# Optimization experiments

Hardware: AMD Instinct MI355X
Metric: run time of the kernel (lower is better)

## Reference

```python
import jax, jax.numpy as jnp
import numpy as np

EMBED = 1024
HEADS = 16
HEAD_DIM = EMBED // HEADS


def setup_inputs() -> dict:
    key = jax.random.key(0)
    ks = jax.random.split(key, 12)
    B, S, E = 2, 2048, EMBED
    scale = 1.0 / np.sqrt(E)
    inp = {
        "query": jax.random.normal(ks[0], (B, S, E), jnp.float32),
        "key": jax.random.normal(ks[1], (B, S, E), jnp.float32),
        "value": jax.random.normal(ks[2], (B, S, E), jnp.float32),
        "Wq": jax.random.normal(ks[3], (E, E), jnp.float32) * scale,
        "bq": jax.random.normal(ks[4], (E,), jnp.float32) * 0.01,
        "Wk": jax.random.normal(ks[5], (E, E), jnp.float32) * scale,
        "bk": jax.random.normal(ks[6], (E,), jnp.float32) * 0.01,
        "Wv": jax.random.normal(ks[7], (E, E), jnp.float32) * scale,
        "bv": jax.random.normal(ks[8], (E,), jnp.float32) * 0.01,
        "Wo": jax.random.normal(ks[9], (E, E), jnp.float32) * scale,
        "bo": jax.random.normal(ks[10], (E,), jnp.float32) * 0.01,
    }
    return inp


def reference(query, key, value, Wq, bq, Wk, bk, Wv, bv, Wo, bo):
    B, Sq, E = query.shape
    Sk = key.shape[1]
    H, D = HEADS, HEAD_DIM
    # QKV projections (torch Linear: x @ W.T + b)
    q = (query @ Wq.T + bq).reshape(B, Sq, H, D)
    k = (key @ Wk.T + bk).reshape(B, Sk, H, D)
    v = (value @ Wv.T + bv).reshape(B, Sk, H, D)
    # energy: [B, H, Sq, Sk]; note scale = 1/sqrt(embed_size), not head_dim
    energy = jnp.einsum("bqhd,bkhd->bhqk", q, k)
    scale = jnp.asarray(E, energy.dtype) ** 0.5
    attn = jax.nn.softmax(energy / scale, axis=-1)
    out = jnp.einsum("bhqk,bkhd->bqhd", attn, v).reshape(B, Sq, E)
    # fc_out (dropout is identity at eval)
    return out @ Wo.T + bo
```

## Files before the change

### kernel.cpp

```cpp
#include <hip/hip_runtime.h>
#include <hip/hip_bf16.h>

typedef __hip_bfloat16 bf16;
typedef short frag8 __attribute__((ext_vector_type(8)));
typedef _Float16 half4 __attribute__((ext_vector_type(4)));
typedef float f32x4 __attribute__((ext_vector_type(4)));

typedef __attribute__((address_space(3))) void lds_void;
typedef __attribute__((address_space(1))) const void gbl_void;

__device__ __forceinline__ void gld16(const void* g, void* l) {
  __builtin_amdgcn_global_load_lds((gbl_void*)g, (lds_void*)l, 16, 0, 0);
}

__device__ __forceinline__ unsigned short f2bf(float f) {
  union { float f; unsigned u; } x; x.f = f;
  unsigned r = x.u + 0x7FFFu + ((x.u >> 16) & 1u);
  return (unsigned short)(r >> 16);
}

#define QSCALE 0.0450842200278f
#define MFIX 4.0f

struct CvtArgs {
  const float4* src[4];
  ushort4* dst[4];
};
__global__ __launch_bounds__(256) void cvt_all(CvtArgs a) {
  const int t = blockIdx.y;
  const int i = blockIdx.x * 256 + threadIdx.x;
  float4 v = a.src[t][i];
  ushort4 o;
  o.x = f2bf(v.x); o.y = f2bf(v.y); o.z = f2bf(v.z); o.w = f2bf(v.w);
  a.dst[t][i] = o;
}

template<int MODE>
__global__ __launch_bounds__(256)
void gemm_bt(const void* __restrict__ A0, const void* __restrict__ A1, const void* __restrict__ A2,
             const bf16* __restrict__ W0, const bf16* __restrict__ W1, const bf16* __restrict__ W2,
             const float* __restrict__ b0, const float* __restrict__ b1, const float* __restrict__ b2,
             void* __restrict__ o0, void* __restrict__ o1, void* __restrict__ o2) {
  constexpr int NK = 1024;
  __shared__ __align__(16) bf16 As[2][128 * 32];
  __shared__ __align__(16) bf16 Bs[2][128 * 32];
  const int tid = threadIdx.x;
  const int wave = tid >> 6, lane = tid & 63, quad = lane >> 4, l16 = lane & 15;
  const int wm = wave >> 1, wn = wave & 1;
  const int bm = blockIdx.x, bn = blockIdx.y;

  const void* A = A0; const bf16* W = W0; const float* bias = b0; void* out = o0;
  int z = 0;
  if constexpr (MODE == 1) {
    z = blockIdx.z;
    if (z == 1) { A = A1; W = W1; bias = b1; out = o1; }
    else if (z == 2) { A = A2; W = W2; bias = b2; out = o2; }
  }

  f32x4 acc[4][4];
  #pragma unroll
  for (int i = 0; i < 4; ++i)
    #pragma unroll
    for (int j = 0; j < 4; ++j)
      acc[i][j] = (f32x4){0.f, 0.f, 0.f, 0.f};

  const bf16* Wb = W + (size_t)bn * 128 * NK;
  const int c0_ = tid & 3, r0_ = tid >> 2;

  auto stageW = [&](int k0, int buf) {
    #pragma unroll
    for (int is = 0; is < 2; ++is) {
      const int c = tid + is * 256;
      const int r = r0_ + is * 64;
      const int gc = (c0_ ^ (r & 3)) << 3;
      gld16(Wb + (size_t)r * NK + k0 + gc, (void*)(&Bs[buf][(size_t)c * 8]));
    }
  };

  const bf16* Ab16 = (const bf16*)A + (size_t)bm * 128 * NK;
  const float* Abf = (const float*)A + (size_t)bm * 128 * NK;
  float4 alo[2], ahi[2];
  auto loadA = [&](int k0, int buf) {
    if constexpr (MODE == 0) {
      #pragma unroll
      for (int is = 0; is < 2; ++is) {
        const int c = tid + is * 256;
        const int r = r0_ + is * 64;
        const int gc = (c0_ ^ (r & 3)) << 3;
        gld16(Ab16 + (size_t)r * NK + k0 + gc, (void*)(&As[buf][(size_t)c * 8]));
      }
    } else {
      #pragma unroll
      for (int is = 0; is < 2; ++is) {
        const int r = r0_ + is * 64;
        const int gc = (c0_ ^ (r & 3)) << 3;
        const float* p = Abf + (size_t)r * NK + k0 + gc;
        alo[is] = *(const float4*)p;
        ahi[is] = *(const float4*)(p + 4);
      }
    }
  };
  auto writeA = [&](int buf) {
    if constexpr (MODE == 1) {
      #pragma unroll
      for (int is = 0; is < 2; ++is) {
        const int c = tid + is * 256;
        ushort4 w0, w1;
        w0.x = f2bf(alo[is].x); w0.y = f2bf(alo[is].y); w0.z = f2bf(alo[is].z); w0.w = f2bf(alo[is].w);
        w1.x = f2bf(ahi[is].x); w1.y = f2bf(ahi[is].y); w1.z = f2bf(ahi[is].z); w1.w = f2bf(ahi[is].w);
        ushort* d = (ushort*)&As[buf][(size_t)c * 8];
        *(ushort4*)d = w0;
        *(ushort4*)(d + 4) = w1;
      }
    }
  };

  loadA(0, 0); stageW(0, 0); writeA(0);
  #pragma unroll 2
  for (int kt = 0; kt < 32; ++kt) {
    __syncthreads();
    if (kt < 31) { loadA((kt + 1) * 32, (kt + 1) & 1); stageW((kt + 1) * 32, (kt + 1) & 1); }
    const bf16* as_ = As[kt & 1];
    const bf16* bs_ = Bs[kt & 1];
    frag8 af[4], bfr[4];
    const int rc = (quad ^ (l16 & 3)) << 3;
    #pragma unroll
    for (int i = 0; i < 4; ++i)
      af[i] = *(const frag8*)&as_[(wm * 64 + i * 16 + l16) * 32 + rc];
    #pragma unroll
    for (int j = 0; j < 4; ++j)
      bfr[j] = *(const frag8*)&bs_[(wn * 64 + j * 16 + l16) * 32 + rc];
    #pragma unroll
    for (int i = 0; i < 4; ++i)
      #pragma unroll
      for (int j = 0; j < 4; ++j)
        acc[i][j] = __builtin_amdgcn_mfma_f32_16x16x32_bf16(af[i], bfr[j], acc[i][j], 0, 0, 0);
    if (kt < 31) writeA((kt + 1) & 1);
  }

  #pragma unroll
  for (int j = 0; j < 4; ++j) {
    const int col = bn * 128 + wn * 64 + j * 16 + l16;
    const float bv = bias[col];
    #pragma unroll
    for (int i = 0; i < 4; ++i) {
      #pragma unroll
      for (int r = 0; r < 4; ++r) {
        const int row = bm * 128 + wm * 64 + i * 16 + quad * 4 + r;
        float v = acc[i][j][r] + bv;
        if constexpr (MODE == 0) {
          ((float*)out)[(size_t)row * 1024 + col] = v;
        } else {
          const int b = row >> 11, s = row & 2047;
          const int hh = col >> 6, d = col & 63;
          const size_t bh = (size_t)(b * 16 + hh);
          if (z == 0) {
            v *= QSCALE;
            ((bf16*)out)[(bh * 2048 + s) * 64 + d] = __float2bfloat16(v);
          } else if (z == 1) {
            const int rr = s & 127;
            const size_t addr = bh * 131072 + (size_t)(s >> 7) * 8192 + (size_t)rr * 64
                              + (size_t)(((d >> 3) ^ (rr & 7)) << 3) + (d & 7);
            ((bf16*)out)[addr] = __float2bfloat16(v);
          } else {
            const int kvl = s & 127;
            const size_t addr = bh * 131072 + (size_t)(s >> 7) * 8192 + (size_t)d * 128
                              + (size_t)((((kvl >> 2) ^ (d & 15)) << 2)) + (kvl & 3);
            ((_Float16*)out)[addr] = (_Float16)v;
          }
        }
      }
    }
  }
}

__global__ __launch_bounds__(256)
void flash_attn(const bf16* __restrict__ Q, const bf16* __restrict__ K,
                const _Float16* __restrict__ Vt, bf16* __restrict__ ctx) {
  __shared__ __align__(16) bf16 Ks[2][128 * 64];
  __shared__ __align__(16) _Float16 Vs[2][64 * 128];
  const int tid = threadIdx.x;
  const int wave = tid >> 6, lane = tid & 63, quad = lane >> 4, l16 = lane & 15;
  const int bh = blockIdx.x, b = bh >> 4, h = bh & 15;
  const int q0 = blockIdx.y * 128 + wave * 32;
  const bf16* Qb = Q + (size_t)bh * 2048 * 64;
  const bf16* Kb = K + (size_t)bh * 131072;
  const _Float16* Vb = Vt + (size_t)bh * 131072;

  frag8 qf[2][2];
  #pragma unroll
  for (int qt = 0; qt < 2; ++qt)
    #pragma unroll
    for (int ks = 0; ks < 2; ++ks)
      qf[qt][ks] = *(const frag8*)(Qb + (size_t)(q0 + qt * 16 + l16) * 64 + ks * 32 + quad * 8);

  f32x4 rsv[2];
  f32x4 o[2][4];
  #pragma unroll
  for (int qt = 0; qt < 2; ++qt) {
    rsv[qt] = (f32x4){0.f, 0.f, 0.f, 0.f};
    #pragma unroll
    for (int dt = 0; dt < 4; ++dt)
      o[qt][dt] = (f32x4){0.f, 0.f, 0.f, 0.f};
  }

  const int xk = l16 & 7;

  auto stage = [&](int kt, int buf) {
    #pragma unroll
    for (int is = 0; is < 4; ++is) {
      const int c = tid + is * 256;
      gld16(Kb + (size_t)kt * 8192 + (size_t)c * 8, (void*)(&Ks[buf][(size_t)c * 8]));
      gld16(Vb + (size_t)kt * 8192 + (size_t)c * 8, (void*)(&Vs[buf][(size_t)c * 8]));
    }
  };

  stage(0, 0);
  #pragma unroll 2
  for (int kt = 0; kt < 16; ++kt) {
    __syncthreads();
    if (kt < 15) stage(kt + 1, (kt + 1) & 1);
    const bf16* ks_ = Ks[kt & 1];
    const _Float16* vs_ = Vs[kt & 1];

    f32x4 s[2][8];
    #pragma unroll
    for (int qt = 0; qt < 2; ++qt)
      #pragma unroll
      for (int jt = 0; jt < 8; ++jt)
        s[qt][jt] = (f32x4){-MFIX, -MFIX, -MFIX, -MFIX};
    #pragma unroll
    for (int ks = 0; ks < 2; ++ks) {
      frag8 kf[8];
      #pragma unroll
      for (int jt = 0; jt < 8; ++jt)
        kf[jt] = *(const frag8*)&ks_[(jt * 16 + l16) * 64 + (((ks * 4 + quad) ^ xk) << 3)];
      #pragma unroll
      for (int qt = 0; qt < 2; ++qt)
        #pragma unroll
        for (int jt = 0; jt < 8; ++jt)
          s[qt][jt] = __builtin_amdgcn_mfma_f32_16x16x32_bf16(kf[jt], qf[qt][ks], s[qt][jt], 0, 0, 0);
    }

    half4 pf[2][8];
    #pragma unroll
    for (int qt = 0; qt < 2; ++qt) {
      #pragma unroll
      for (int jt = 0; jt < 8; ++jt) {
        f32x4 p4;
        #pragma unroll
        for (int r = 0; r < 4; ++r)
          p4[r] = __builtin_amdgcn_exp2f(s[qt][jt][r]);
        rsv[qt] += p4;
        #pragma unroll
        for (int r = 0; r < 4; ++r)
          pf[qt][jt][r] = (_Float16)p4[r];
      }
    }

    #pragma unroll
    for (int jt = 0; jt < 8; ++jt) {
      half4 vf[4];
      #pragma unroll
      for (int dt = 0; dt < 4; ++dt)
        vf[dt] = *(const half4*)&vs_[(dt * 16 + l16) * 128 + (((jt * 4 + quad) ^ l16) << 2)];
      #pragma unroll
      for (int qt = 0; qt < 2; ++qt)
        #pragma unroll
        for (int dt = 0; dt < 4; ++dt)
          o[qt][dt] = __builtin_amdgcn_mfma_f32_16x16x16f16(vf[dt], pf[qt][jt], o[qt][dt], 0, 0, 0);
    }
  }

  #pragma unroll
  for (int qt = 0; qt < 2; ++qt) {
    float l = rsv[qt][0] + rsv[qt][1] + rsv[qt][2] + rsv[qt][3];
    l += __shfl_xor(l, 16, 64);
    l += __shfl_xor(l, 32, 64);
    const float inv = __builtin_amdgcn_rcpf(l);
    const int q = q0 + qt * 16 + l16;
    #pragma unroll
    for (int dt = 0; dt < 4; ++dt) {
      ushort4 w;
      w.x = f2bf(o[qt][dt][0] * inv);
      w.y = f2bf(o[qt][dt][1] * inv);
      w.z = f2bf(o[qt][dt][2] * inv);
      w.w = f2bf(o[qt][dt][3] * inv);
      const int d = dt * 16 + quad * 4;
      *(uint2*)&ctx[((size_t)(b * 2048 + q)) * 1024 + h * 64 + d] = *(uint2*)&w;
    }
  }
}

extern "C" void kernel_launch(void* const* d_in, const int* in_sizes, int n_in,
                              void* d_out, int out_size, void* d_ws, size_t ws_size,
                              hipStream_t stream) {
  const float* q_in = (const float*)d_in[0];
  const float* k_in = (const float*)d_in[1];
  const float* v_in = (const float*)d_in[2];
  const float* Wq = (const float*)d_in[3];
  const float* bq = (const float*)d_in[4];
  const float* Wk = (const float*)d_in[5];
  const float* bk = (const float*)d_in[6];
  const float* Wv = (const float*)d_in[7];
  const float* bv = (const float*)d_in[8];
  const float* Wo = (const float*)d_in[9];
  const float* bo = (const float*)d_in[10];

  char* ws = (char*)d_ws;
  const size_t MB = 1024 * 1024;
  bf16* Wqb = (bf16*)(ws + 0 * MB);
  bf16* Wkb = (bf16*)(ws + 2 * MB);
  bf16* Wvb = (bf16*)(ws + 4 * MB);
  bf16* Wob = (bf16*)(ws + 6 * MB);
  bf16* Qw  = (bf16*)(ws + 8 * MB);
  bf16* Kw  = (bf16*)(ws + 16 * MB);
  _Float16* Vtw = (_Float16*)(ws + 24 * MB);
  bf16* Ctx = (bf16*)(ws + 32 * MB);

  {
    CvtArgs a;
    a.src[0] = (const float4*)Wq; a.dst[0] = (ushort4*)Wqb;
    a.src[1] = (const float4*)Wk; a.dst[1] = (ushort4*)Wkb;
    a.src[2] = (const float4*)Wv; a.dst[2] = (ushort4*)Wvb;
    a.src[3] = (const float4*)Wo; a.dst[3] = (ushort4*)Wob;
    cvt_all<<<dim3(1024, 4), 256, 0, stream>>>(a);
  }

  gemm_bt<1><<<dim3(32, 8, 3), 256, 0, stream>>>(q_in, k_in, v_in, Wqb, Wkb, Wvb,
                                                 bq, bk, bv, Qw, Kw, (void*)Vtw);
  flash_attn<<<dim3(32, 16), 256, 0, stream>>>(Qw, Kw, Vtw, Ctx);
  gemm_bt<0><<<dim3(32, 8, 1), 256, 0, stream>>>(Ctx, nullptr, nullptr, Wob, nullptr, nullptr,
                                                 bo, nullptr, nullptr, d_out, nullptr, nullptr);
}
```

Measured before the change: 250.5 us.

## Halve output GEMM tile height and deepen fp32 A prefetch in QKV GEMM

The output projection GEMM now uses 64-row tiles with each wave owning 16 rows across all 128 columns, doubling the grid from 256 to 512 blocks so more of the GPU's compute units get work. The QKV projection GEMM gains a two-deep register prefetch of the fp32 A tiles, loading two k-steps ahead and converting one step ahead, to hide global-load latency behind the MFMAs. The trade-offs are less data reuse per block in the output GEMM and higher register pressure in the QKV GEMM.

```diff
diff --git a/kernel.cpp b/kernel.cpp
--- a/kernel.cpp
+++ b/kernel.cpp
@@ -42,7 +42,8 @@
              const float* __restrict__ b0, const float* __restrict__ b1, const float* __restrict__ b2,
              void* __restrict__ o0, void* __restrict__ o1, void* __restrict__ o2) {
   constexpr int NK = 1024;
-  __shared__ __align__(16) bf16 As[2][128 * 32];
+  constexpr int BM = (MODE == 1) ? 128 : 64;
+  __shared__ __align__(16) bf16 As[2][BM * 32];
   __shared__ __align__(16) bf16 Bs[2][128 * 32];
   const int tid = threadIdx.x;
   const int wave = tid >> 6, lane = tid & 63, quad = lane >> 4, l16 = lane & 15;
@@ -57,13 +58,6 @@
     else if (z == 2) { A = A2; W = W2; bias = b2; out = o2; }
   }
 
-  f32x4 acc[4][4];
-  #pragma unroll
-  for (int i = 0; i < 4; ++i)
-    #pragma unroll
-    for (int j = 0; j < 4; ++j)
-      acc[i][j] = (f32x4){0.f, 0.f, 0.f, 0.f};
-
   const bf16* Wb = W + (size_t)bn * 128 * NK;
   const int c0_ = tid & 3, r0_ = tid >> 2;
 
@@ -77,80 +71,116 @@
     }
   };
 
-  const bf16* Ab16 = (const bf16*)A + (size_t)bm * 128 * NK;
-  const float* Abf = (const float*)A + (size_t)bm * 128 * NK;
-  float4 alo[2], ahi[2];
-  auto loadA = [&](int k0, int buf) {
-    if constexpr (MODE == 0) {
-      #pragma unroll
-      for (int is = 0; is < 2; ++is) {
-        const int c = tid + is * 256;
-        const int r = r0_ + is * 64;
-        const int gc = (c0_ ^ (r & 3)) << 3;
-        gld16(Ab16 + (size_t)r * NK + k0 + gc, (void*)(&As[buf][(size_t)c * 8]));
-      }
-    } else {
+  const int rc = (quad ^ (l16 & 3)) << 3;
+
+  if constexpr (MODE == 0) {
+    const bf16* Ab16 = (const bf16*)A + (size_t)bm * 64 * NK;
+    f32x4 acc[8];
+    #pragma unroll
+    for (int j = 0; j < 8; ++j) acc[j] = (f32x4){0.f, 0.f, 0.f, 0.f};
+
+    auto stageA = [&](int k0, int buf) {
+      const int r = r0_;
+      const int gc = (c0_ ^ (r & 3)) << 3;
+      gld16(Ab16 + (size_t)r * NK + k0 + gc, (void*)(&As[buf][(size_t)tid * 8]));
+    };
+
+    stageA(0, 0); stageW(0, 0);
+    #pragma unroll 2
+    for (int kt = 0; kt < 32; ++kt) {
+      __syncthreads();
+      if (kt < 31) { stageA((kt + 1) * 32, (kt + 1) & 1); stageW((kt + 1) * 32, (kt + 1) & 1); }
+      const bf16* as_ = As[kt & 1];
+      const bf16* bs_ = Bs[kt & 1];
+      frag8 af = *(const frag8*)&as_[(wave * 16 + l16) * 32 + rc];
+      #pragma unroll
+      for (int j = 0; j < 8; ++j) {
+        frag8 bf_ = *(const frag8*)&bs_[(j * 16 + l16) * 32 + rc];
+        acc[j] = __builtin_amdgcn_mfma_f32_16x16x32_bf16(af, bf_, acc[j], 0, 0, 0);
+      }
+    }
+    #pragma unroll
+    for (int j = 0; j < 8; ++j) {
+      const int col = bn * 128 + j * 16 + l16;
+      const float bv = bias[col];
+      #pragma unroll
+      for (int r = 0; r < 4; ++r) {
+        const int row = bm * 64 + wave * 16 + quad * 4 + r;
+        ((float*)out)[(size_t)row * 1024 + col] = acc[j][r] + bv;
+      }
+    }
+  } else {
+    const float* Abf = (const float*)A + (size_t)bm * 128 * NK;
+    f32x4 acc[4][4];
+    #pragma unroll
+    for (int i = 0; i < 4; ++i)
+      #pragma unroll
+      for (int j = 0; j < 4; ++j)
+        acc[i][j] = (f32x4){0.f, 0.f, 0.f, 0.f};
+
+    float4 alo[2][2], ahi[2][2];
+    auto loadA = [&](int k0, int set) {
       #pragma unroll
       for (int is = 0; is < 2; ++is) {
         const int r = r0_ + is * 64;
         const int gc = (c0_ ^ (r & 3)) << 3;
         const float* p = Abf + (size_t)r * NK + k0 + gc;
-        alo[is] = *(const float4*)p;
-        ahi[is] = *(const float4*)(p + 4);
-      }
-    }
-  };
-  auto writeA = [&](int buf) {
-    if constexpr (MODE == 1) {
+        alo[set][is] = *(const float4*)p;
+        ahi[set][is] = *(const float4*)(p + 4);
+      }
+    };
+    auto writeA = [&](int set, int buf) {
       #pragma unroll
       for (int is = 0; is < 2; ++is) {
         const int c = tid + is * 256;
         ushort4 w0, w1;
-        w0.x = f2bf(alo[is].x); w0.y = f2bf(alo[is].y); w0.z = f2bf(alo[is].z); w0.w = f2bf(alo[is].w);
-        w1.x = f2bf(ahi[is].x); w1.y = f2bf(ahi[is].y); w1.z = f2bf(ahi[is].z); w1.w = f2bf(ahi[is].w);
+        w0.x = f2bf(alo[set][is].x); w0.y = f2bf(alo[set][is].y);
+        w0.z = f2bf(alo[set][is].z); w0.w = f2bf(alo[set][is].w);
+        w1.x = f2bf(ahi[set][is].x); w1.y = f2bf(ahi[set][is].y);
+        w1.z = f2bf(ahi[set][is].z); w1.w = f2bf(ahi[set][is].w);
         ushort* d = (ushort*)&As[buf][(size_t)c * 8];
         *(ushort4*)d = w0;
         *(ushort4*)(d + 4) = w1;
       }
-    }
-  };
-
-  loadA(0, 0); stageW(0, 0); writeA(0);
-  #pragma unroll 2
-  for (int kt = 0; kt < 32; ++kt) {
-    __syncthreads();
-    if (kt < 31) { loadA((kt + 1) * 32, (kt + 1) & 1); stageW((kt + 1) * 32, (kt + 1) & 1); }
-    const bf16* as_ = As[kt & 1];
-    const bf16* bs_ = Bs[kt & 1];
-    frag8 af[4], bfr[4];
-    const int rc = (quad ^ (l16 & 3)) << 3;
-    #pragma unroll
-    for (int i = 0; i < 4; ++i)
-      af[i] = *(const frag8*)&as_[(wm * 64 + i * 16 + l16) * 32 + rc];
-    #pragma unroll
-    for (int j = 0; j < 4; ++j)
-      bfr[j] = *(const frag8*)&bs_[(wn * 64 + j * 16 + l16) * 32 + rc];
-    #pragma unroll
-    for (int i = 0; i < 4; ++i)
+    };
+
+    loadA(0, 0); stageW(0, 0);
+    writeA(0, 0);
+    loadA(32, 1);
+    #pragma unroll 2
+    for (int kt = 0; kt < 32; ++kt) {
+      __syncthreads();
+      if (kt < 31) {
+        stageW((kt + 1) * 32, (kt + 1) & 1);
+        writeA((kt + 1) & 1, (kt + 1) & 1);
+      }
+      if (kt < 30) loadA((kt + 2) * 32, kt & 1);
+      const bf16* as_ = As[kt & 1];
+      const bf16* bs_ = Bs[kt & 1];
+      frag8 af[4], bfr[4];
+      #pragma unroll
+      for (int i = 0; i < 4; ++i)
+        af[i] = *(const frag8*)&as_[(wm * 64 + i * 16 + l16) * 32 + rc];
       #pragma unroll
       for (int j = 0; j < 4; ++j)
-        acc[i][j] = __builtin_amdgcn_mfma_f32_16x16x32_bf16(af[i], bfr[j], acc[i][j], 0, 0, 0);
-    if (kt < 31) writeA((kt + 1) & 1);
-  }
-
-  #pragma unroll
-  for (int j = 0; j < 4; ++j) {
-    const int col = bn * 128 + wn * 64 + j * 16 + l16;
-    const float bv = bias[col];
-    #pragma unroll
-    for (int i = 0; i < 4; ++i) {
-      #pragma unroll
-      for (int r = 0; r < 4; ++r) {
-        const int row = bm * 128 + wm * 64 + i * 16 + quad * 4 + r;
-        float v = acc[i][j][r] + bv;
-        if constexpr (MODE == 0) {
-          ((float*)out)[(size_t)row * 1024 + col] = v;
-        } else {
+        bfr[j] = *(const frag8*)&bs_[(wn * 64 + j * 16 + l16) * 32 + rc];
+      #pragma unroll
+      for (int i = 0; i < 4; ++i)
+        #pragma unroll
+        for (int j = 0; j < 4; ++j)
+          acc[i][j] = __builtin_amdgcn_mfma_f32_16x16x32_bf16(af[i], bfr[j], acc[i][j], 0, 0, 0);
+    }
+
+    #pragma unroll
+    for (int j = 0; j < 4; ++j) {
+      const int col = bn * 128 + wn * 64 + j * 16 + l16;
+      const float bv = bias[col];
+      #pragma unroll
+      for (int i = 0; i < 4; ++i) {
+        #pragma unroll
+        for (int r = 0; r < 4; ++r) {
+          const int row = bm * 128 + wm * 64 + i * 16 + quad * 4 + r;
+          float v = acc[i][j][r] + bv;
           const int b = row >> 11, s = row & 2047;
           const int hh = col >> 6, d = col & 63;
           const size_t bh = (size_t)(b * 16 + hh);
@@ -330,6 +360,6 @@
   gemm_bt<1><<<dim3(32, 8, 3), 256, 0, stream>>>(q_in, k_in, v_in, Wqb, Wkb, Wvb,
                                                  bq, bk, bv, Qw, Kw, (void*)Vtw);
   flash_attn<<<dim3(32, 16), 256, 0, stream>>>(Qw, Kw, Vtw, Ctx);
-  gemm_bt<0><<<dim3(32, 8, 1), 256, 0, stream>>>(Ctx, nullptr, nullptr, Wob, nullptr, nullptr,
+  gemm_bt<0><<<dim3(64, 8, 1), 256, 0, stream>>>(Ctx, nullptr, nullptr, Wob, nullptr, nullptr,
                                                  bo, nullptr, nullptr, d_out, nullptr, nullptr);
 }
```

After: 253.5 us. No clear change (+1.2%).
